# Optimization experiments

Measured on AMD Instinct MI355X. Metric: run time of the kernel, lower is better.

Reference implementation:

```python
import math
import jax, jax.numpy as jnp
import numpy as np

B, N, C_IN, C_OUT = 16, 1024, 256, 256


def setup_inputs() -> dict:
    key = jax.random.key(0)
    k_x, k_q, k_k, k_v, k_s, k_e = jax.random.split(key, 6)
    x = jax.random.normal(k_x, (B, N, C_IN), dtype=jnp.float32)
    # torch Linear(in, out, bias=False) == x @ W with W: [in, out]
    sc = 1.0 / math.sqrt(C_IN)
    W_q = jax.random.normal(k_q, (C_IN, C_OUT), dtype=jnp.float32) * sc
    W_k = jax.random.normal(k_k, (C_IN, C_OUT), dtype=jnp.float32) * sc
    W_v = jax.random.normal(k_v, (C_IN, C_OUT), dtype=jnp.float32) * sc
    W_sigma = jax.random.normal(k_s, (C_IN, 1), dtype=jnp.float32) * sc
    # fixed standard-normal noise replacing torch.normal's on-the-fly sampling
    eps = jax.random.normal(k_e, (B, N, N), dtype=jnp.float32)
    return {"x": x, "W_q": W_q, "W_k": W_k, "W_v": W_v,
            "W_sigma": W_sigma, "eps": eps}


def reference(x, W_q, W_k, W_v, W_sigma, eps):
    n = x.shape[1]
    d_model = W_q.shape[1]
    Q = x @ W_q            # [B, n, d]
    K = x @ W_k            # [B, n, d]
    V = x @ W_v            # [B, n, d]
    sigma = x @ W_sigma    # [B, n, 1]

    # prior association: gaussian = Normal(mean=|i-j|, std=|sigma|), row-normalized
    idx = jnp.arange(n)
    p = jnp.abs(idx[:, None] - idx[None, :]).astype(x.dtype)   # [n, n]
    gaussian = p[None, :, :] + jnp.abs(sigma) * eps            # [B, n, n]
    P = gaussian / jnp.sum(gaussian, axis=-1, keepdims=True)

    # series association: softmax over dim=0 (batch), exactly as the torch code
    scores = jnp.einsum('bnd,bmd->bnm', Q, K) / math.sqrt(d_model)
    S = jax.nn.softmax(scores, axis=0)

    Z = jnp.einsum('bnm,bmd->bnd', S, V)                       # reconstruction
    return Z, P, S
```

## Files before the change

kernel.cpp:

```cpp
#include <hip/hip_runtime.h>
#include <hip/hip_bf16.h>
#include <math.h>

#define B_ 16
#define N_ 1024
#define C_ 256

typedef unsigned short ushort_t;
typedef __attribute__((ext_vector_type(8))) short short8;
typedef __attribute__((ext_vector_type(4))) float f32x4;

static __device__ __forceinline__ ushort_t f2bf(float f) {
    __hip_bfloat16 h = __float2bfloat16(f);
    return *(ushort_t*)&h;
}

static __device__ __forceinline__ float bf2f(ushort_t u) {
    return __uint_as_float(((unsigned int)u) << 16);
}

static __device__ __forceinline__ void async16(const ushort_t* g, ushort_t* l) {
    __builtin_amdgcn_global_load_lds(
        (const __attribute__((address_space(1))) unsigned int*)g,
        (__attribute__((address_space(3))) unsigned int*)l,
        16, 0, 0);
}

template <int OUT_BF16>
__global__ __launch_bounds__(256) void gemm_nt_bf16(
    const ushort_t* __restrict__ A, const ushort_t* __restrict__ B,
    void* __restrict__ Cp, int M, int N, int K,
    long sA, long sB, long sC, float alpha)
{
    A += (long)blockIdx.z * sA;
    B += (long)blockIdx.z * sB;

    __shared__ ushort_t sh[2][2 * 128 * 32];
    float* shF = (float*)sh;

    const int tid  = threadIdx.x;
    const int wave = tid >> 6;
    const int lane = tid & 63;
    const int wm   = wave >> 1;
    const int wn   = wave & 1;
    const int row0 = blockIdx.y * 128;
    const int col0 = blockIdx.x * 128;

    const int r_grp = lane >> 2;
    const int c_chk = lane & 3;
    const int swz   = c_chk ^ ((r_grp >> 1) & 3);
    const int ga0 = wave * 2, ga1 = wave * 2 + 1;

    const ushort_t* agp0 = A + (long)(row0 + ga0 * 16 + r_grp) * K + swz * 8;
    const ushort_t* agp1 = A + (long)(row0 + ga1 * 16 + r_grp) * K + swz * 8;
    const ushort_t* bgp0 = B + (long)(col0 + ga0 * 16 + r_grp) * K + swz * 8;
    const ushort_t* bgp1 = B + (long)(col0 + ga1 * 16 + r_grp) * K + swz * 8;

    const int lr16 = lane & 15;
    const int q16  = lane >> 4;
    const int slot = (q16 ^ ((lr16 >> 1) & 3)) * 8;

    f32x4 acc[4][4] = {};

    {
        ushort_t* As = sh[0];
        ushort_t* Bs = sh[0] + 128 * 32;
        async16(agp0, &As[ga0 * 512]);
        async16(agp1, &As[ga1 * 512]);
        async16(bgp0, &Bs[ga0 * 512]);
        async16(bgp1, &Bs[ga1 * 512]);
    }
    __syncthreads();

    int p = 0;
    for (int k0 = 0; k0 < K; k0 += 32) {
        if (k0 + 32 < K) {
            ushort_t* As = sh[p ^ 1];
            ushort_t* Bs = sh[p ^ 1] + 128 * 32;
            async16(agp0 + k0 + 32, &As[ga0 * 512]);
            async16(agp1 + k0 + 32, &As[ga1 * 512]);
            async16(bgp0 + k0 + 32, &Bs[ga0 * 512]);
            async16(bgp1 + k0 + 32, &Bs[ga1 * 512]);
        }

        const ushort_t* As = sh[p];
        const ushort_t* Bs = sh[p] + 128 * 32;
        short8 av[4], bv[4];
#pragma unroll
        for (int i = 0; i < 4; i++)
            av[i] = *(const short8*)&As[(wm * 64 + i * 16 + lr16) * 32 + slot];
#pragma unroll
        for (int j = 0; j < 4; j++)
            bv[j] = *(const short8*)&Bs[(wn * 64 + j * 16 + lr16) * 32 + slot];

#pragma unroll
        for (int i = 0; i < 4; i++)
#pragma unroll
            for (int j = 0; j < 4; j++)
                acc[i][j] = __builtin_amdgcn_mfma_f32_16x16x32_bf16(
                    av[i], bv[j], acc[i][j], 0, 0, 0);

        __syncthreads();
        p ^= 1;
    }

#pragma unroll
    for (int i = 0; i < 4; i++) {
#pragma unroll
        for (int j = 0; j < 4; j++) {
            const int rl = wm * 16 + q16 * 4;
            const int cl = wn * 64 + j * 16 + lr16;
#pragma unroll
            for (int r = 0; r < 4; r++) {
                const int rr = rl + r;
                const int xr = ((rr >> 2) & 1) << 4;
                shF[rr * 128 + (cl ^ xr)] = alpha * acc[i][j][r];
            }
        }
        __syncthreads();

        if constexpr (OUT_BF16) {
            ushort_t* C = (ushort_t*)Cp + (long)blockIdx.z * sC;
#pragma unroll
            for (int v = 0; v < 2; v++) {
                const int idx = v * 256 + tid;
                const int rl = idx >> 4;
                const int c8 = idx & 15;
                const int xr4 = ((rl >> 2) & 1) << 2;
                const int gr = row0 + (rl >> 4) * 64 + i * 16 + (rl & 15);
                const float4 a = ((const float4*)(shF + rl * 128))[(c8 * 2) ^ xr4];
                const float4 b = ((const float4*)(shF + rl * 128))[(c8 * 2 + 1) ^ xr4];
                short8 pk;
                pk[0] = (short)f2bf(a.x); pk[1] = (short)f2bf(a.y);
                pk[2] = (short)f2bf(a.z); pk[3] = (short)f2bf(a.w);
                pk[4] = (short)f2bf(b.x); pk[5] = (short)f2bf(b.y);
                pk[6] = (short)f2bf(b.z); pk[7] = (short)f2bf(b.w);
                *(short8*)(C + (long)gr * N + col0 + c8 * 8) = pk;
            }
        } else {
            float* C = (float*)Cp + (long)blockIdx.z * sC;
#pragma unroll
            for (int v = 0; v < 4; v++) {
                const int idx = v * 256 + tid;
                const int rl = idx >> 5;
                const int c4 = idx & 31;
                const int xr4 = ((rl >> 2) & 1) << 2;
                const int gr = row0 + (rl >> 4) * 64 + i * 16 + (rl & 15);
                const float4 val = ((const float4*)(shF + rl * 128))[c4 ^ xr4];
                *(float4*)(C + (long)gr * N + col0 + c4 * 4) = val;
            }
        }
        __syncthreads();
    }
}

__global__ __launch_bounds__(256) void cast_fused(
    const float* __restrict__ x, ushort_t* __restrict__ xbf,
    const float* __restrict__ Wq, const float* __restrict__ Wk,
    const float* __restrict__ Wv, ushort_t* __restrict__ WbfT,
    const float* __restrict__ Wsig, float* __restrict__ asig)
{
    __shared__ float t[32][33];
    const int blk = blockIdx.x;
    if (blk < 4096) {
        const long i = ((long)blk * 256 + threadIdx.x) * 4;
        const float4 v = *(const float4*)(x + i);
        ushort4 o;
        o.x = f2bf(v.x); o.y = f2bf(v.y); o.z = f2bf(v.z); o.w = f2bf(v.w);
        *(ushort4*)(xbf + i) = o;
        if (asig) {
            const int lane = threadIdx.x & 63;
            const float4 w = *(const float4*)(Wsig + lane * 4);
            float d = v.x * w.x + v.y * w.y + v.z * w.z + v.w * w.w;
#pragma unroll
            for (int off = 32; off; off >>= 1) d += __shfl_down(d, off, 64);
            if (lane == 0) asig[blk * 4 + (threadIdx.x >> 6)] = fabsf(d);
        }
    } else {
        const int m = blk - 4096;
        const float* W = ((m >> 6) == 0) ? Wq : ((m >> 6) == 1) ? Wk : Wv;
        const int rem = m & 63;
        const int n0 = (rem & 7) * 32, k0 = (rem >> 3) * 32;
        const int tx = threadIdx.x & 31, ty = threadIdx.x >> 5;
#pragma unroll
        for (int j = 0; j < 4; j++)
            t[ty + j * 8][tx] = W[(long)(k0 + ty + j * 8) * 256 + n0 + tx];
        __syncthreads();
        ushort_t* o = WbfT + (long)(m >> 6) * 65536;
#pragma unroll
        for (int j = 0; j < 4; j++)
            o[(long)(n0 + ty + j * 8) * 256 + k0 + tx] = f2bf(t[tx][ty + j * 8]);
    }
}

__global__ __launch_bounds__(256) void transpose_v_kernel(
    const ushort_t* __restrict__ V, ushort_t* __restrict__ VT)
{
    __shared__ ushort_t t[32][33];
    const long NC = (long)N_ * C_;
    const ushort_t* Vb = V + (long)blockIdx.z * NC;
    ushort_t* Tb = VT + (long)blockIdx.z * NC;
    const int n0 = blockIdx.x * 32, m0 = blockIdx.y * 32;
    const int tx = threadIdx.x & 31, ty = threadIdx.x >> 5;
#pragma unroll
    for (int j = 0; j < 4; j++)
        t[ty + j * 8][tx] = Vb[(long)(m0 + ty + j * 8) * C_ + n0 + tx];
    __syncthreads();
#pragma unroll
    for (int j = 0; j < 4; j++)
        Tb[(long)(n0 + ty + j * 8) * N_ + m0 + tx] = t[tx][ty + j * 8];
}

__global__ __launch_bounds__(256) void softmax_batch(
    ushort_t* __restrict__ Sc, float* __restrict__ S)
{
    const long NN = (long)N_ * N_;
    const long i4 = ((long)blockIdx.x * 256 + threadIdx.x) * 4;

    float4 v[B_];
    float mx = -INFINITY, my = -INFINITY, mz = -INFINITY, mw = -INFINITY;
#pragma unroll
    for (int b = 0; b < B_; b++) {
        const ushort4 u = *(const ushort4*)(Sc + (long)b * NN + i4);
        v[b].x = bf2f(u.x); v[b].y = bf2f(u.y);
        v[b].z = bf2f(u.z); v[b].w = bf2f(u.w);
        mx = fmaxf(mx, v[b].x); my = fmaxf(my, v[b].y);
        mz = fmaxf(mz, v[b].z); mw = fmaxf(mw, v[b].w);
    }
    float sx = 0.f, sy = 0.f, sz = 0.f, sw = 0.f;
#pragma unroll
    for (int b = 0; b < B_; b++) {
        v[b].x = __expf(v[b].x - mx); sx += v[b].x;
        v[b].y = __expf(v[b].y - my); sy += v[b].y;
        v[b].z = __expf(v[b].z - mz); sz += v[b].z;
        v[b].w = __expf(v[b].w - mw); sw += v[b].w;
    }
    const float ix = 1.0f / sx, iy = 1.0f / sy, iz = 1.0f / sz, iw = 1.0f / sw;
#pragma unroll
    for (int b = 0; b < B_; b++) {
        float4 o;
        o.x = v[b].x * ix; o.y = v[b].y * iy;
        o.z = v[b].z * iz; o.w = v[b].w * iw;
        *(float4*)(S + (long)b * NN + i4) = o;
        ushort4 ob;
        ob.x = f2bf(o.x); ob.y = f2bf(o.y); ob.z = f2bf(o.z); ob.w = f2bf(o.w);
        *(ushort4*)(Sc + (long)b * NN + i4) = ob;
    }
}

__device__ __forceinline__ float block_reduce_sum(float v, float* red)
{
#pragma unroll
    for (int off = 32; off; off >>= 1) v += __shfl_down(v, off, 64);
    __syncthreads();
    if ((threadIdx.x & 63) == 0) red[threadIdx.x >> 6] = v;
    __syncthreads();
    return red[0] + red[1] + red[2] + red[3];
}

__global__ __launch_bounds__(256) void p_kernel(
    const float* __restrict__ x, const float* __restrict__ Wsig,
    const float* __restrict__ eps, float* __restrict__ P,
    const float* __restrict__ asig)
{
    __shared__ float red[4];
    const int bn = blockIdx.x;
    const int n = bn & (N_ - 1);
    const int tid = threadIdx.x;

    float a;
    if (asig) {
        a = asig[bn];
    } else {
        a = fabsf(block_reduce_sum(x[(long)bn * C_ + tid] * Wsig[tid], red));
    }

    const float* erow = eps + (long)bn * N_;
    const float4 e = *(const float4*)(erow + tid * 4);
    const int j0 = tid * 4;
    const float g0 = (float)abs(n - (j0 + 0)) + a * e.x;
    const float g1 = (float)abs(n - (j0 + 1)) + a * e.y;
    const float g2 = (float)abs(n - (j0 + 2)) + a * e.z;
    const float g3 = (float)abs(n - (j0 + 3)) + a * e.w;

    const float total = block_reduce_sum(g0 + g1 + g2 + g3, red);
    const float inv = 1.0f / total;

    float4 o;
    o.x = g0 * inv; o.y = g1 * inv; o.z = g2 * inv; o.w = g3 * inv;
    *(float4*)(P + (long)bn * N_ + j0) = o;
}

extern "C" void kernel_launch(void* const* d_in, const int* in_sizes, int n_in,
                              void* d_out, int out_size, void* d_ws, size_t ws_size,
                              hipStream_t stream)
{
    const float* x    = (const float*)d_in[0];
    const float* Wq   = (const float*)d_in[1];
    const float* Wk   = (const float*)d_in[2];
    const float* Wv   = (const float*)d_in[3];
    const float* Wsig = (const float*)d_in[4];
    const float* eps  = (const float*)d_in[5];
    float* out = (float*)d_out;

    const long ZN = (long)B_ * N_ * C_;
    const long PN = (long)B_ * N_ * N_;
    const long NC = (long)N_ * C_;
    const long NN = (long)N_ * N_;

    float* Zp = out;
    float* Pp = out + ZN;
    float* Sp = out + ZN + PN;

    ushort_t* base = (ushort_t*)Pp;
    ushort_t* Qbf  = base;
    ushort_t* Kbf  = base + ZN;
    ushort_t* Vbf  = base + 2 * ZN;
    ushort_t* xbf  = base + 3 * ZN;
    ushort_t* VbfT = base + 3 * ZN;
    ushort_t* WbfT = base + 4 * ZN;
    ushort_t* Scbf = base + 4 * ZN;

    float* asig = (ws_size >= (size_t)(B_ * N_) * sizeof(float))
                      ? (float*)d_ws : nullptr;

    const dim3 blk(256);

    cast_fused<<<dim3(4096 + 192), blk, 0, stream>>>(
        x, xbf, Wq, Wk, Wv, WbfT, Wsig, asig);

    gemm_nt_bf16<1><<<dim3(2, 128, 3), blk, 0, stream>>>(
        xbf, WbfT, Qbf, B_ * N_, C_, C_, 0, 65536, ZN, 1.0f);

    transpose_v_kernel<<<dim3(8, 32, 16), blk, 0, stream>>>(Vbf, VbfT);

    gemm_nt_bf16<1><<<dim3(8, 8, 16), blk, 0, stream>>>(
        Qbf, Kbf, Scbf, N_, N_, C_, NC, NC, NN, 0.0625f);

    softmax_batch<<<dim3(NN / 1024), blk, 0, stream>>>(Scbf, Sp);

    gemm_nt_bf16<0><<<dim3(2, 8, 16), blk, 0, stream>>>(
        Scbf, VbfT, Zp, N_, C_, N_, NN, NC, NC, 1.0f);

    p_kernel<<<dim3(B_ * N_), blk, 0, stream>>>(x, Wsig, eps, Pp, asig);
}
```

Measured before the change: 287.9 us.

## Use 512-thread GEMM blocks with XCD swizzle and wave-per-row P kernel

The bf16 GEMM now runs with 8 waves per block. Each wave owns a 64x32 sub-tile instead of 64x64, which halves accumulators and global-to-LDS loads per thread. Workgroup IDs are remapped so consecutive tiles land on the same XCD for better L2 locality. The P kernel processes one row per wave with shuffle-only reductions, removing block-level syncs and shared memory. The trade-offs are more waves contending for LDS and barriers, and a swizzle that assumes the workgroup count is divisible by 8.

Result: faster. 280.5 us (-2.5%).

```diff
diff --git a/kernel.cpp b/kernel.cpp
--- a/kernel.cpp
+++ b/kernel.cpp
@@ -26,14 +26,26 @@
         16, 0, 0);
 }
 
-template <int OUT_BF16>
-__global__ __launch_bounds__(256) void gemm_nt_bf16(
+template <int OUT_BF16, int SWZ>
+__global__ __launch_bounds__(512) void gemm_nt_bf16(
     const ushort_t* __restrict__ A, const ushort_t* __restrict__ B,
     void* __restrict__ Cp, int M, int N, int K,
     long sA, long sB, long sC, float alpha)
 {
-    A += (long)blockIdx.z * sA;
-    B += (long)blockIdx.z * sB;
+    int bx = blockIdx.x, by = blockIdx.y, bz = blockIdx.z;
+    if constexpr (SWZ) {
+        const int gx = gridDim.x, gy = gridDim.y;
+        const int nwg = gx * gy * (int)gridDim.z;
+        const int lid = bx + gx * (by + gy * bz);
+        const int cpx = nwg >> 3;
+        const int s = (lid & 7) * cpx + (lid >> 3);
+        bx = s % gx;
+        const int t = s / gx;
+        by = t % gy;
+        bz = t / gy;
+    }
+    A += (long)bz * sA;
+    B += (long)bz * sB;
 
     __shared__ ushort_t sh[2][2 * 128 * 32];
     float* shF = (float*)sh;
@@ -41,34 +53,29 @@
     const int tid  = threadIdx.x;
     const int wave = tid >> 6;
     const int lane = tid & 63;
-    const int wm   = wave >> 1;
-    const int wn   = wave & 1;
-    const int row0 = blockIdx.y * 128;
-    const int col0 = blockIdx.x * 128;
+    const int wm   = wave >> 2;
+    const int wn   = wave & 3;
+    const int row0 = by * 128;
+    const int col0 = bx * 128;
 
     const int r_grp = lane >> 2;
     const int c_chk = lane & 3;
     const int swz   = c_chk ^ ((r_grp >> 1) & 3);
-    const int ga0 = wave * 2, ga1 = wave * 2 + 1;
-
-    const ushort_t* agp0 = A + (long)(row0 + ga0 * 16 + r_grp) * K + swz * 8;
-    const ushort_t* agp1 = A + (long)(row0 + ga1 * 16 + r_grp) * K + swz * 8;
-    const ushort_t* bgp0 = B + (long)(col0 + ga0 * 16 + r_grp) * K + swz * 8;
-    const ushort_t* bgp1 = B + (long)(col0 + ga1 * 16 + r_grp) * K + swz * 8;
+
+    const ushort_t* agp = A + (long)(row0 + wave * 16 + r_grp) * K + swz * 8;
+    const ushort_t* bgp = B + (long)(col0 + wave * 16 + r_grp) * K + swz * 8;
 
     const int lr16 = lane & 15;
     const int q16  = lane >> 4;
     const int slot = (q16 ^ ((lr16 >> 1) & 3)) * 8;
 
-    f32x4 acc[4][4] = {};
+    f32x4 acc[4][2] = {};
 
     {
         ushort_t* As = sh[0];
         ushort_t* Bs = sh[0] + 128 * 32;
-        async16(agp0, &As[ga0 * 512]);
-        async16(agp1, &As[ga1 * 512]);
-        async16(bgp0, &Bs[ga0 * 512]);
-        async16(bgp1, &Bs[ga1 * 512]);
+        async16(agp, &As[wave * 512]);
+        async16(bgp, &Bs[wave * 512]);
     }
     __syncthreads();
 
@@ -77,26 +84,24 @@
         if (k0 + 32 < K) {
             ushort_t* As = sh[p ^ 1];
             ushort_t* Bs = sh[p ^ 1] + 128 * 32;
-            async16(agp0 + k0 + 32, &As[ga0 * 512]);
-            async16(agp1 + k0 + 32, &As[ga1 * 512]);
-            async16(bgp0 + k0 + 32, &Bs[ga0 * 512]);
-            async16(bgp1 + k0 + 32, &Bs[ga1 * 512]);
+            async16(agp + k0 + 32, &As[wave * 512]);
+            async16(bgp + k0 + 32, &Bs[wave * 512]);
         }
 
         const ushort_t* As = sh[p];
         const ushort_t* Bs = sh[p] + 128 * 32;
-        short8 av[4], bv[4];
+        short8 av[4], bv[2];
 #pragma unroll
         for (int i = 0; i < 4; i++)
             av[i] = *(const short8*)&As[(wm * 64 + i * 16 + lr16) * 32 + slot];
 #pragma unroll
-        for (int j = 0; j < 4; j++)
-            bv[j] = *(const short8*)&Bs[(wn * 64 + j * 16 + lr16) * 32 + slot];
+        for (int j = 0; j < 2; j++)
+            bv[j] = *(const short8*)&Bs[(wn * 32 + j * 16 + lr16) * 32 + slot];
 
 #pragma unroll
         for (int i = 0; i < 4; i++)
 #pragma unroll
-            for (int j = 0; j < 4; j++)
+            for (int j = 0; j < 2; j++)
                 acc[i][j] = __builtin_amdgcn_mfma_f32_16x16x32_bf16(
                     av[i], bv[j], acc[i][j], 0, 0, 0);
 
@@ -107,9 +112,9 @@
 #pragma unroll
     for (int i = 0; i < 4; i++) {
 #pragma unroll
-        for (int j = 0; j < 4; j++) {
+        for (int j = 0; j < 2; j++) {
             const int rl = wm * 16 + q16 * 4;
-            const int cl = wn * 64 + j * 16 + lr16;
+            const int cl = wn * 32 + j * 16 + lr16;
 #pragma unroll
             for (int r = 0; r < 4; r++) {
                 const int rr = rl + r;
@@ -120,28 +125,25 @@
         __syncthreads();
 
         if constexpr (OUT_BF16) {
-            ushort_t* C = (ushort_t*)Cp + (long)blockIdx.z * sC;
+            ushort_t* C = (ushort_t*)Cp + (long)bz * sC;
+            const int idx = tid;
+            const int rl = idx >> 4;
+            const int c8 = idx & 15;
+            const int xr4 = ((rl >> 2) & 1) << 2;
+            const int gr = row0 + (rl >> 4) * 64 + i * 16 + (rl & 15);
+            const float4 a = ((const float4*)(shF + rl * 128))[(c8 * 2) ^ xr4];
+            const float4 b = ((const float4*)(shF + rl * 128))[(c8 * 2 + 1) ^ xr4];
+            short8 pk;
+            pk[0] = (short)f2bf(a.x); pk[1] = (short)f2bf(a.y);
+            pk[2] = (short)f2bf(a.z); pk[3] = (short)f2bf(a.w);
+            pk[4] = (short)f2bf(b.x); pk[5] = (short)f2bf(b.y);
+            pk[6] = (short)f2bf(b.z); pk[7] = (short)f2bf(b.w);
+            *(short8*)(C + (long)gr * N + col0 + c8 * 8) = pk;
+        } else {
+            float* C = (float*)Cp + (long)bz * sC;
 #pragma unroll
             for (int v = 0; v < 2; v++) {
-                const int idx = v * 256 + tid;
-                const int rl = idx >> 4;
-                const int c8 = idx & 15;
-                const int xr4 = ((rl >> 2) & 1) << 2;
-                const int gr = row0 + (rl >> 4) * 64 + i * 16 + (rl & 15);
-                const float4 a = ((const float4*)(shF + rl * 128))[(c8 * 2) ^ xr4];
-                const float4 b = ((const float4*)(shF + rl * 128))[(c8 * 2 + 1) ^ xr4];
-                short8 pk;
-                pk[0] = (short)f2bf(a.x); pk[1] = (short)f2bf(a.y);
-                pk[2] = (short)f2bf(a.z); pk[3] = (short)f2bf(a.w);
-                pk[4] = (short)f2bf(b.x); pk[5] = (short)f2bf(b.y);
-                pk[6] = (short)f2bf(b.z); pk[7] = (short)f2bf(b.w);
-                *(short8*)(C + (long)gr * N + col0 + c8 * 8) = pk;
-            }
-        } else {
-            float* C = (float*)Cp + (long)blockIdx.z * sC;
-#pragma unroll
-            for (int v = 0; v < 4; v++) {
-                const int idx = v * 256 + tid;
+                const int idx = v * 512 + tid;
                 const int rl = idx >> 5;
                 const int c4 = idx & 31;
                 const int xr4 = ((rl >> 2) & 1) << 2;
@@ -248,47 +250,52 @@
     }
 }
 
-__device__ __forceinline__ float block_reduce_sum(float v, float* red)
-{
-#pragma unroll
-    for (int off = 32; off; off >>= 1) v += __shfl_down(v, off, 64);
-    __syncthreads();
-    if ((threadIdx.x & 63) == 0) red[threadIdx.x >> 6] = v;
-    __syncthreads();
-    return red[0] + red[1] + red[2] + red[3];
-}
-
 __global__ __launch_bounds__(256) void p_kernel(
     const float* __restrict__ x, const float* __restrict__ Wsig,
     const float* __restrict__ eps, float* __restrict__ P,
     const float* __restrict__ asig)
 {
-    __shared__ float red[4];
-    const int bn = blockIdx.x;
-    const int n = bn & (N_ - 1);
-    const int tid = threadIdx.x;
+    const int row  = blockIdx.x * 4 + (threadIdx.x >> 6);
+    const int lane = threadIdx.x & 63;
+    const int n = row & (N_ - 1);
 
     float a;
     if (asig) {
-        a = asig[bn];
+        a = asig[row];
     } else {
-        a = fabsf(block_reduce_sum(x[(long)bn * C_ + tid] * Wsig[tid], red));
-    }
-
-    const float* erow = eps + (long)bn * N_;
-    const float4 e = *(const float4*)(erow + tid * 4);
-    const int j0 = tid * 4;
-    const float g0 = (float)abs(n - (j0 + 0)) + a * e.x;
-    const float g1 = (float)abs(n - (j0 + 1)) + a * e.y;
-    const float g2 = (float)abs(n - (j0 + 2)) + a * e.z;
-    const float g3 = (float)abs(n - (j0 + 3)) + a * e.w;
-
-    const float total = block_reduce_sum(g0 + g1 + g2 + g3, red);
-    const float inv = 1.0f / total;
-
-    float4 o;
-    o.x = g0 * inv; o.y = g1 * inv; o.z = g2 * inv; o.w = g3 * inv;
-    *(float4*)(P + (long)bn * N_ + j0) = o;
+        const float4 xv = *(const float4*)(x + (long)row * C_ + lane * 4);
+        const float4 wv = *(const float4*)(Wsig + lane * 4);
+        float d = xv.x * wv.x + xv.y * wv.y + xv.z * wv.z + xv.w * wv.w;
+#pragma unroll
+        for (int off = 32; off; off >>= 1) d += __shfl_xor(d, off, 64);
+        a = fabsf(d);
+    }
+
+    const float4* erow = (const float4*)(eps + (long)row * N_);
+    float4 e[4], g[4];
+    float sum = 0.f;
+#pragma unroll
+    for (int k = 0; k < 4; k++) {
+        e[k] = erow[k * 64 + lane];
+        const int j0 = (k * 64 + lane) * 4;
+        g[k].x = (float)abs(n - (j0 + 0)) + a * e[k].x;
+        g[k].y = (float)abs(n - (j0 + 1)) + a * e[k].y;
+        g[k].z = (float)abs(n - (j0 + 2)) + a * e[k].z;
+        g[k].w = (float)abs(n - (j0 + 3)) + a * e[k].w;
+        sum += g[k].x + g[k].y + g[k].z + g[k].w;
+    }
+#pragma unroll
+    for (int off = 32; off; off >>= 1) sum += __shfl_xor(sum, off, 64);
+    const float inv = 1.0f / sum;
+
+    float4* prow = (float4*)(P + (long)row * N_);
+#pragma unroll
+    for (int k = 0; k < 4; k++) {
+        float4 o;
+        o.x = g[k].x * inv; o.y = g[k].y * inv;
+        o.z = g[k].z * inv; o.w = g[k].w * inv;
+        prow[k * 64 + lane] = o;
+    }
 }
 
 extern "C" void kernel_launch(void* const* d_in, const int* in_sizes, int n_in,
@@ -325,22 +332,23 @@
                       ? (float*)d_ws : nullptr;
 
     const dim3 blk(256);
+    const dim3 blk512(512);
 
     cast_fused<<<dim3(4096 + 192), blk, 0, stream>>>(
         x, xbf, Wq, Wk, Wv, WbfT, Wsig, asig);
 
-    gemm_nt_bf16<1><<<dim3(2, 128, 3), blk, 0, stream>>>(
+    gemm_nt_bf16<1, 1><<<dim3(2, 128, 3), blk512, 0, stream>>>(
         xbf, WbfT, Qbf, B_ * N_, C_, C_, 0, 65536, ZN, 1.0f);
 
     transpose_v_kernel<<<dim3(8, 32, 16), blk, 0, stream>>>(Vbf, VbfT);
 
-    gemm_nt_bf16<1><<<dim3(8, 8, 16), blk, 0, stream>>>(
+    gemm_nt_bf16<1, 1><<<dim3(8, 8, 16), blk512, 0, stream>>>(
         Qbf, Kbf, Scbf, N_, N_, C_, NC, NC, NN, 0.0625f);
 
     softmax_batch<<<dim3(NN / 1024), blk, 0, stream>>>(Scbf, Sp);
 
-    gemm_nt_bf16<0><<<dim3(2, 8, 16), blk, 0, stream>>>(
+    gemm_nt_bf16<0, 1><<<dim3(2, 8, 16), blk512, 0, stream>>>(
         Scbf, VbfT, Zp, N_, C_, N_, NN, NC, NC, 1.0f);
 
-    p_kernel<<<dim3(B_ * N_), blk, 0, stream>>>(x, Wsig, eps, Pp, asig);
-}
+    p_kernel<<<dim3((B_ * N_) / 4), blk, 0, stream>>>(x, Wsig, eps, Pp, asig);
+}
```
